# Kernel tuning notes

Measured on AMD Instinct MI355X. Metric: run time of the kernel, lower is better.

## Reference

```python
import jax, jax.numpy as jnp
import numpy as np

B, C, HH, WW, QK = 8, 64, 64, 64, 8


def setup_inputs() -> dict:
    key = jax.random.key(0)
    ks = jax.random.split(key, 22)
    s = 0.05
    def W(k, o, i):
        return jax.random.normal(k, (o, i), jnp.float32) * s
    def bvec(k, o):
        return jax.random.normal(k, (o,), jnp.float32) * s
    return {
        "H_in": jax.random.normal(ks[0], (B, C, HH, WW), jnp.float32),
        "M_prev": jax.random.normal(ks[1], (B, C, HH, WW), jnp.float32),
        "wq": W(ks[2], QK, C), "bq": bvec(ks[3], QK),
        "wkh": W(ks[4], QK, C), "bkh": bvec(ks[5], QK),
        "wvh": W(ks[6], C, C), "bvh": bvec(ks[7], C),
        "wkm": W(ks[8], QK, C), "bkm": bvec(ks[9], QK),
        "wvm": W(ks[10], C, C), "bvm": bvec(ks[11], C),
        "wz": W(ks[12], C, 2 * C), "bz": bvec(ks[13], C),
        "wo": W(ks[14], C, 2 * C), "bo": bvec(ks[15], C),
        "wg": W(ks[16], C, 2 * C), "bg": bvec(ks[17], C),
        "wi": W(ks[18], C, 2 * C), "bi": bvec(ks[19], C),
    }


def _conv1x1(w, b, x):
    # x: [B, Cin, N] -> [B, Cout, N]
    return jnp.einsum("oc,bcn->bon", w, x) + b[None, :, None]


def reference(H_in, M_prev, wq, bq, wkh, bkh, wvh, bvh, wkm, bkm, wvm, bvm,
              wz, bz, wo, bo, wg, bg, wi, bi):
    Bn, Cn, Hn, Wn = H_in.shape
    N = Hn * Wn
    h = H_in.reshape(Bn, Cn, N)   # flatten spatial
    m = M_prev.reshape(Bn, Cn, N)

    Q = _conv1x1(wq, bq, h)       # [B, QK, N]
    Kh = _conv1x1(wkh, bkh, h)
    Vh = _conv1x1(wvh, bvh, h)    # [B, C, N]
    Km = _conv1x1(wkm, bkm, m)
    Vm = _conv1x1(wvm, bvm, m)

    scale = jnp.asarray(np.sqrt(Q.shape[1]), Q.dtype)
    # scores: [B, N, N], softmax over last axis
    Ah = jax.nn.softmax(jnp.einsum("bcn,bcm->bnm", Q, Kh) / scale, axis=-1)
    Am = jax.nn.softmax(jnp.einsum("bcn,bcm->bnm", Q, Km) / scale, axis=-1)
    # Zh = Vh @ Ah^T : [B, C, N]
    Zh = jnp.einsum("bcm,bnm->bcn", Vh, Ah)
    Zm = jnp.einsum("bcm,bnm->bcn", Vm, Am)

    Z = _conv1x1(wz, bz, jnp.concatenate([Zh, Zm], axis=1))  # [B, C, N]
    concat = jnp.concatenate([h, Z], axis=1)                  # [B, 2C, N]
    O_t = jax.nn.sigmoid(_conv1x1(wo, bo, concat))
    G_t = jnp.tanh(_conv1x1(wg, bg, concat))
    I_t = jax.nn.sigmoid(_conv1x1(wi, bi, concat))

    M_t = (1.0 - I_t) * m + I_t * G_t
    H_out = O_t * M_t
    return (H_out.reshape(Bn, Cn, Hn, Wn), M_t.reshape(Bn, Cn, Hn, Wn))
```

## Files before the change

kernel.cpp:

```cpp
#include <hip/hip_runtime.h>

#define BATCH 8
#define CC 64
#define NN 4096
#define SCL 0.51006973f

typedef __attribute__((ext_vector_type(8))) short s16x8;
typedef __attribute__((ext_vector_type(4))) short s16x4;
typedef __attribute__((ext_vector_type(4))) float f32x4;
typedef __attribute__((ext_vector_type(2))) unsigned int uint2v;

__device__ __forceinline__ short f2bf(float f) {
  unsigned u = __builtin_bit_cast(unsigned, f);
  u += 0x7fffu + ((u >> 16) & 1u);
  return (short)(u >> 16);
}
__device__ __forceinline__ float bf2f(short h) {
  unsigned u = ((unsigned)(unsigned short)h) << 16;
  return __builtin_bit_cast(float, u);
}
__device__ __forceinline__ unsigned cvt_pk_bf16(float lo, float hi) {
  unsigned r;
  asm volatile("v_cvt_pk_bf16_f32 %0, %1, %2" : "=v"(r) : "v"(lo), "v"(hi));
  return r;
}

__device__ __forceinline__ int kperm(int kk) {
  int hh = (kk >> 5) & 1, g = (kk >> 3) & 3, c = kk & 7;
  return hh * 32 + (c < 4 ? (g << 2) + c : 16 + ((g ^ 2) << 2) + (c - 4));
}

__global__ void prep_weights_kernel(const float* __restrict__ wz, const float* __restrict__ bz,
                                    const float* __restrict__ wo, const float* __restrict__ bo,
                                    const float* __restrict__ wg, const float* __restrict__ bg,
                                    const float* __restrict__ wi, const float* __restrict__ bi,
                                    const float* __restrict__ wq, const float* __restrict__ bq,
                                    const float* __restrict__ wkh, const float* __restrict__ bkh,
                                    const float* __restrict__ wvh, const float* __restrict__ bvh,
                                    const float* __restrict__ wkm, const float* __restrict__ bkm,
                                    const float* __restrict__ wvm, const float* __restrict__ bvm,
                                    short* __restrict__ Weff, float* __restrict__ beff,
                                    short* __restrict__ Wcat, float* __restrict__ bias) {
  int i = blockIdx.x * 256 + threadIdx.x;
  const float* wjs[3] = {wo, wg, wi};
  const float* bjs[3] = {bo, bg, bi};
  const float gsc[3] = {1.44269504f, 2.88539008f, 1.44269504f};
  if (i < 36864) {
    int j = i / 12288, rem = i % 12288, o = rem / 192, k = rem % 192;
    const float* wj = wjs[j];
    float v;
    if (k < 64) {
      v = wj[o * 128 + k];
    } else {
      v = 0.f;
      #pragma unroll 8
      for (int t = 0; t < 64; ++t) v += wj[o * 128 + 64 + t] * wz[t * 128 + (k - 64)];
    }
    Weff[i] = f2bf(v * gsc[j]);
  } else if (i < 37056) {
    int i2 = i - 36864;
    int j = i2 >> 6, o = i2 & 63;
    const float* wj = wjs[j];
    float v = bjs[j][o];
    #pragma unroll 8
    for (int t = 0; t < 64; ++t) v += wj[o * 128 + 64 + t] * bz[t];
    beff[i2] = v * gsc[j];
  } else if (i < 47296) {
    int i2 = i - 37056;
    int src = i2 / 5120, rem = i2 % 5120, row = rem >> 6, col = rem & 63;
    float v;
    if (src == 0) {
      if (row < 64) v = wvh[row * 64 + col];
      else if (row < 72) v = wq[(row - 64) * 64 + col] * SCL;
      else v = wkh[(row - 72) * 64 + col];
    } else {
      if (row < 64) v = wvm[row * 64 + col];
      else if (row < 72) v = wkm[(row - 64) * 64 + col];
      else v = 0.f;
    }
    Wcat[i2] = f2bf(v);
  } else if (i < 47456) {
    int i3 = i - 47296;
    int src = i3 / 80, row = i3 % 80;
    float v;
    if (src == 0) v = (row < 64) ? bvh[row] : (row < 72 ? bq[row - 64] * SCL : bkh[row - 72]);
    else          v = (row < 64) ? bvm[row] : (row < 72 ? bkm[row - 64] : 0.f);
    bias[i3] = v;
  }
}

__global__ __launch_bounds__(256) void proj_kernel(
    const float* __restrict__ H_in, const float* __restrict__ M_prev,
    const short* __restrict__ Wcat, const float* __restrict__ bias,
    short* __restrict__ Qt, short* __restrict__ Kht, short* __restrict__ Kmt,
    short* __restrict__ Vh, short* __restrict__ Vm, short* __restrict__ Ht) {
  int src = blockIdx.x & 1;
  int n0 = ((blockIdx.x >> 1) & 31) << 7;
  int b = blockIdx.x >> 6;
  int tid = threadIdx.x, w = tid >> 6, l = tid & 63, lg = l >> 4, ll = l & 15;

  const float* __restrict__ X = src ? M_prev : H_in;
  short* __restrict__ Vp = src ? Vm : Vh;

  __shared__ __align__(16) short Xt[128][68];

  {
    int nl = tid & 127, chalf = (tid >> 7) << 5;
    int n = n0 + nl;
    #pragma unroll
    for (int cg = 0; cg < 8; ++cg) {
      int c = chalf + cg * 4;
      float v0 = X[((size_t)((b << 6) + c + 0)) * NN + n];
      float v1 = X[((size_t)((b << 6) + c + 1)) * NN + n];
      float v2 = X[((size_t)((b << 6) + c + 2)) * NN + n];
      float v3 = X[((size_t)((b << 6) + c + 3)) * NN + n];
      uint2v pk;
      pk.x = cvt_pk_bf16(v0, v1);
      pk.y = cvt_pk_bf16(v2, v3);
      *(uint2v*)&Xt[nl][c] = pk;
    }
  }
  __syncthreads();

  if (src == 0) {
    #pragma unroll
    for (int j = 0; j < 4; ++j) {
      int ci = tid + j * 256;
      int n = ci >> 3, seg = ci & 7;
      *(s16x8*)(Ht + ((size_t)(b * NN + n0 + n)) * 64 + seg * 8) = *(const s16x8*)&Xt[n][seg * 8];
    }
  }

  f32x4 acc[5][2];
  #pragma unroll
  for (int ot = 0; ot < 5; ++ot)
    #pragma unroll
    for (int ns = 0; ns < 2; ++ns)
      #pragma unroll
      for (int r = 0; r < 4; ++r) acc[ot][ns][r] = bias[src * 80 + ot * 16 + lg * 4 + r];

  #pragma unroll
  for (int kk = 0; kk < 2; ++kk) {
    s16x8 aw[5];
    #pragma unroll
    for (int ot = 0; ot < 5; ++ot)
      aw[ot] = *(const s16x8*)(Wcat + ((size_t)(src * 80 + ot * 16 + ll)) * 64 + kk * 32 + lg * 8);
    #pragma unroll
    for (int ns = 0; ns < 2; ++ns) {
      s16x8 bx = *(const s16x8*)&Xt[w * 32 + ns * 16 + ll][kk * 32 + lg * 8];
      #pragma unroll
      for (int ot = 0; ot < 5; ++ot)
        acc[ot][ns] = __builtin_amdgcn_mfma_f32_16x16x32_bf16(aw[ot], bx, acc[ot][ns], 0, 0, 0);
    }
  }

  #pragma unroll
  for (int ns = 0; ns < 2; ++ns) {
    int n = n0 + w * 32 + ns * 16 + ll;
    #pragma unroll
    for (int ot = 0; ot < 4; ++ot) {
      #pragma unroll
      for (int r = 0; r < 4; ++r) {
        int o = ot * 16 + lg * 4 + r;
        Vp[((size_t)((b << 6) + o)) * NN + n] = f2bf(acc[ot][ns][r]);
      }
    }
    int pr = (n & ~63) + kperm(n & 63);
    #pragma unroll
    for (int r = 0; r < 4; ++r) {
      float v = acc[4][ns][r];
      if (src == 0) {
        if (lg < 2) Qt[((size_t)(b * NN + n)) * 8 + (lg * 4 + r)] = f2bf(v);
        else        Kht[((size_t)(b * NN + pr)) * 8 + ((lg - 2) * 4 + r)] = f2bf(v);
      } else {
        if (lg < 2) Kmt[((size_t)(b * NN + pr)) * 8 + (lg * 4 + r)] = f2bf(v);
      }
    }
  }
}

__global__ __launch_bounds__(256, 6) void attn_kernel(
    const short* __restrict__ Qt, const short* __restrict__ Kht, const short* __restrict__ Kmt,
    const short* __restrict__ Vh, const short* __restrict__ Vm,
    short* __restrict__ Zp, float* __restrict__ dnb) {
  unsigned vb = (blockIdx.x & 7) * 256 + (blockIdx.x >> 3);
  int kh = vb >> 10;
  int b  = (vb >> 7) & 7;
  int s  = (vb >> 6) & 1;
  int q0 = (vb & 63) << 6;
  int tid = threadIdx.x;
  int w = tid >> 6, l = tid & 63, lg = l >> 4, ll = l & 15;
  const bool lo32 = (l < 32);

  const short* __restrict__ Kp = s ? Kmt : Kht;
  const short* __restrict__ Vp = s ? Vm : Vh;

  __shared__ __align__(16) short Vt[2][64][64];
  __shared__ __align__(16) short Ktl[2][64][8];
  short* VtF = &Vt[0][0][0];
  short* KtF = &Ktl[0][0][0];

  s16x8 bq = {};
  if (lg == 0) bq = *(const s16x8*)(Qt + ((size_t)(b * NN + q0 + w * 16 + ll)) * 8);
  s16x8 ones;
  #pragma unroll
  for (int i = 0; i < 8; ++i) ones[i] = (short)0x3F80;

  f32x4 accZ[4];
  f32x4 accDn = {0.f, 0.f, 0.f, 0.f};
  #pragma unroll
  for (int cs = 0; cs < 4; ++cs) accZ[cs] = (f32x4){0.f, 0.f, 0.f, 0.f};

  const int vOff0 = ll * 64 + ((lg ^ (ll & 7)) << 3);
  const int vOff1 = ll * 64 + (((lg ^ 4) ^ (ll & 7)) << 3);
  const int kOff  = ll * 8;

  const int row0 = w * 8 + (l >> 3);
  const int swz  = ((l & 7) ^ (l >> 3)) << 3;
  const short* vsrc0 = Vp + ((size_t)((b << 6) + row0)) * NN + kh * 2048 + swz;
  const short* vsrc1 = Vp + ((size_t)((b << 6) + 32 + row0)) * NN + kh * 2048 + swz;
  const short* ksrc  = Kp + ((size_t)(b * NN) + kh * 2048 + l) * 8;

#define GLDS(src_, dst_) \
  __builtin_amdgcn_global_load_lds((const __attribute__((address_space(1))) void*)(src_), \
                                   (__attribute__((address_space(3))) void*)(dst_), 16, 0, 0)
#define STAGE(bufL, ktL) do { \
    GLDS(vsrc0 + (ktL) * 64, VtF + (bufL) * 4096 + w * 512); \
    GLDS(vsrc1 + (ktL) * 64, VtF + (bufL) * 4096 + 2048 + w * 512); \
    if (w == 0) GLDS(ksrc + (ktL) * 512, KtF + (bufL) * 512); \
  } while (0)

  auto compute = [&](int bufL) {
    float p[4][4];
    #pragma unroll
    for (int hh = 0; hh < 2; ++hh) {
      #pragma unroll
      for (int par = 0; par < 2; ++par) {
        s16x8 ak = *(const s16x8*)(KtF + bufL * 512 + (hh * 32 + par * 16) * 8 + kOff);
        f32x4 sc = __builtin_amdgcn_mfma_f32_16x16x32_bf16(ak, bq, (f32x4){0.f,0.f,0.f,0.f}, 0, 0, 0);
        #pragma unroll
        for (int r = 0; r < 4; ++r) p[hh * 2 + par][r] = __builtin_amdgcn_exp2f(sc[r]);
      }
    }
    unsigned wkv[4][2];
    #pragma unroll
    for (int ks = 0; ks < 4; ++ks) {
      wkv[ks][0] = cvt_pk_bf16(p[ks][0], p[ks][1]);
      wkv[ks][1] = cvt_pk_bf16(p[ks][2], p[ks][3]);
    }
    #pragma unroll
    for (int hh = 0; hh < 2; ++hh) {
      unsigned o0 = wkv[hh * 2 + 1][0], o1 = wkv[hh * 2 + 1][1];
      uint2v pr0 = __builtin_amdgcn_permlane32_swap(o0, o0, false, false);
      uint2v pr1 = __builtin_amdgcn_permlane32_swap(o1, o1, false, false);
      unsigned sw0 = lo32 ? pr0.y : pr0.x;
      unsigned sw1 = lo32 ? pr1.y : pr1.x;
      union { unsigned u[4]; s16x8 v; } bpu;
      bpu.u[0] = wkv[hh * 2][0];
      bpu.u[1] = wkv[hh * 2][1];
      bpu.u[2] = sw0;
      bpu.u[3] = sw1;
      s16x8 bp = bpu.v;
      accDn = __builtin_amdgcn_mfma_f32_16x16x32_bf16(ones, bp, accDn, 0, 0, 0);
      const int vo = hh ? vOff1 : vOff0;
      #pragma unroll
      for (int cs = 0; cs < 4; ++cs) {
        s16x8 av = *(const s16x8*)(VtF + bufL * 4096 + cs * 1024 + vo);
        accZ[cs] = __builtin_amdgcn_mfma_f32_16x16x32_bf16(av, bp, accZ[cs], 0, 0, 0);
      }
    }
  };

  STAGE(0, 0);
  #pragma unroll 1
  for (int kt2 = 0; kt2 < 16; ++kt2) {
    int kt = kt2 * 2;
    asm volatile("s_waitcnt vmcnt(0)" ::: "memory");
    __builtin_amdgcn_s_barrier();
    STAGE(1, kt + 1);
    compute(0);
    asm volatile("s_waitcnt vmcnt(0)" ::: "memory");
    __builtin_amdgcn_s_barrier();
    if (kt2 < 15) STAGE(0, kt + 2);
    compute(1);
  }

  #pragma unroll
  for (int cs = 0; cs < 4; ++cs) {
    s16x4 o4;
    #pragma unroll
    for (int r = 0; r < 4; ++r) o4[r] = f2bf(accZ[cs][r]);
    *(s16x4*)(Zp + ((size_t)((kh * 8 + b) * NN + q0 + w * 16 + ll)) * 128 + s * 64 + cs * 16 + lg * 4) = o4;
  }
  if (l < 16)
    dnb[((size_t)(kh * 16 + b * 2 + s)) * NN + q0 + w * 16 + l] = accDn[0];
#undef STAGE
#undef GLDS
}

__global__ __launch_bounds__(256) void gates_kernel(
    const float* __restrict__ M_prev, const short* __restrict__ Ht,
    const short* __restrict__ Zp, const float* __restrict__ dnb,
    const short* __restrict__ Weff, const float* __restrict__ beff,
    float* __restrict__ out) {
  int b = blockIdx.x >> 7;
  int n0 = (blockIdx.x & 127) << 5;
  int tid = threadIdx.x, w = tid >> 6, l = tid & 63, lg = l >> 4, ll = l & 15;
  __shared__ __align__(16) short Xt[32][200];

  {
    int n = tid >> 3, seg = tid & 7;
    *(s16x8*)&Xt[n][seg * 8] = *(const s16x8*)(Ht + ((size_t)(b * NN + n0 + n)) * 64 + seg * 8);
  }
  {
    int n = tid >> 3, cq = tid & 7, sidx = cq >> 2;
    const short* z0 = Zp + ((size_t)(b * NN + n0 + n)) * 128 + cq * 16;
    const short* z1 = Zp + ((size_t)((8 + b) * NN + n0 + n)) * 128 + cq * 16;
    float d0 = dnb[((size_t)(b * 2 + sidx)) * NN + n0 + n];
    float d1 = dnb[((size_t)(16 + b * 2 + sidx)) * NN + n0 + n];
    float rd = __builtin_amdgcn_rcpf(d0 + d1);
    s16x8 a0 = *(const s16x8*)z0;
    s16x8 a1 = *(const s16x8*)z1;
    s16x8 b0 = *(const s16x8*)(z0 + 8);
    s16x8 b1 = *(const s16x8*)(z1 + 8);
    s16x8 o0, o1;
    #pragma unroll
    for (int j = 0; j < 8; ++j) {
      o0[j] = f2bf((bf2f(a0[j]) + bf2f(a1[j])) * rd);
      o1[j] = f2bf((bf2f(b0[j]) + bf2f(b1[j])) * rd);
    }
    *(s16x8*)&Xt[n][64 + cq * 16] = o0;
    *(s16x8*)&Xt[n][64 + cq * 16 + 8] = o1;
  }
  __syncthreads();

  f32x4 acc[3][2];
  #pragma unroll
  for (int j = 0; j < 3; ++j)
    #pragma unroll
    for (int ns = 0; ns < 2; ++ns)
      #pragma unroll
      for (int r = 0; r < 4; ++r) acc[j][ns][r] = beff[j * 64 + w * 16 + lg * 4 + r];

  #pragma unroll
  for (int kk = 0; kk < 6; ++kk) {
    s16x8 aw[3];
    #pragma unroll
    for (int j = 0; j < 3; ++j)
      aw[j] = *(const s16x8*)(Weff + ((size_t)(j * 64 + w * 16 + ll)) * 192 + kk * 32 + lg * 8);
    #pragma unroll
    for (int ns = 0; ns < 2; ++ns) {
      s16x8 bx = *(const s16x8*)&Xt[ns * 16 + ll][kk * 32 + lg * 8];
      #pragma unroll
      for (int j = 0; j < 3; ++j)
        acc[j][ns] = __builtin_amdgcn_mfma_f32_16x16x32_bf16(aw[j], bx, acc[j][ns], 0, 0, 0);
    }
  }

  float* Hout = out;
  float* Mout = out + (size_t)BATCH * CC * NN;
  #pragma unroll
  for (int ns = 0; ns < 2; ++ns) {
    #pragma unroll
    for (int r = 0; r < 4; ++r) {
      int c = w * 16 + lg * 4 + r;
      int n = n0 + ns * 16 + ll;
      size_t idx = ((size_t)((b << 6) + c)) * NN + n;
      float xo = acc[0][ns][r], xg = acc[1][ns][r], xi = acc[2][ns][r];
      float o  = __builtin_amdgcn_rcpf(1.f + __builtin_amdgcn_exp2f(-xo));
      float g  = 2.f * __builtin_amdgcn_rcpf(1.f + __builtin_amdgcn_exp2f(-xg)) - 1.f;
      float ii = __builtin_amdgcn_rcpf(1.f + __builtin_amdgcn_exp2f(-xi));
      float m  = M_prev[idx];
      float mt = (1.f - ii) * m + ii * g;
      Mout[idx] = mt;
      Hout[idx] = o * mt;
    }
  }
}

extern "C" void kernel_launch(void* const* d_in, const int* in_sizes, int n_in,
                              void* d_out, int out_size, void* d_ws, size_t ws_size,
                              hipStream_t stream) {
  (void)in_sizes; (void)n_in; (void)out_size; (void)ws_size;
  const float* H_in  = (const float*)d_in[0];
  const float* M_prev= (const float*)d_in[1];
  const float* wq  = (const float*)d_in[2];
  const float* bq  = (const float*)d_in[3];
  const float* wkh = (const float*)d_in[4];
  const float* bkh = (const float*)d_in[5];
  const float* wvh = (const float*)d_in[6];
  const float* bvh = (const float*)d_in[7];
  const float* wkm = (const float*)d_in[8];
  const float* bkm = (const float*)d_in[9];
  const float* wvm = (const float*)d_in[10];
  const float* bvm = (const float*)d_in[11];
  const float* wz  = (const float*)d_in[12];
  const float* bz  = (const float*)d_in[13];
  const float* wo  = (const float*)d_in[14];
  const float* bo  = (const float*)d_in[15];
  const float* wg  = (const float*)d_in[16];
  const float* bg  = (const float*)d_in[17];
  const float* wi  = (const float*)d_in[18];
  const float* bi  = (const float*)d_in[19];

  char* ws = (char*)d_ws;
  size_t off = 0;
  auto alloc = [&](size_t bytes) -> void* {
    void* p = ws + off;
    off += (bytes + 255) & ~(size_t)255;
    return p;
  };
  short* Weff = (short*)alloc(3 * 64 * 192 * 2);
  float* beff = (float*)alloc(192 * 4);
  short* Wcat = (short*)alloc(2 * 80 * 64 * 2);
  float* bias = (float*)alloc(160 * 4);
  short* Qt   = (short*)alloc((size_t)BATCH * NN * 8 * 2);
  short* Kht  = (short*)alloc((size_t)BATCH * NN * 8 * 2);
  short* Kmt  = (short*)alloc((size_t)BATCH * NN * 8 * 2);
  short* Vh   = (short*)alloc((size_t)BATCH * CC * NN * 2);
  short* Vm   = (short*)alloc((size_t)BATCH * CC * NN * 2);
  short* Ht   = (short*)alloc((size_t)BATCH * NN * 64 * 2);
  short* Zp   = (short*)alloc((size_t)2 * BATCH * NN * 128 * 2);
  float* dnb  = (float*)alloc((size_t)2 * BATCH * 2 * NN * 4);

  prep_weights_kernel<<<186, 256, 0, stream>>>(wz, bz, wo, bo, wg, bg, wi, bi,
                                               wq, bq, wkh, bkh, wvh, bvh, wkm, bkm, wvm, bvm,
                                               Weff, beff, Wcat, bias);
  proj_kernel<<<512, 256, 0, stream>>>(H_in, M_prev, Wcat, bias, Qt, Kht, Kmt, Vh, Vm, Ht);
  attn_kernel<<<2048, 256, 0, stream>>>(Qt, Kht, Kmt, Vh, Vm, Zp, dnb);
  gates_kernel<<<1024, 256, 0, stream>>>(M_prev, Ht, Zp, dnb, Weff, beff, (float*)d_out);
}
```

Measured before the change: 189.7 us.

## Vectorize projection I/O via LDS staging, drop Ht buffer, raise attn occupancy

The projection kernel now handles 64-column tiles with 1024 blocks. It reads inputs as float4 and transposes them into LDS. Its V outputs are staged through a shared tile so they go out as 16-byte coalesced stores instead of scattered 2-byte writes. The bf16 copy of H (Ht) is removed, and the gates kernel re-reads H_in in fp32 and converts it itself. The attention kernel's launch bounds are raised to 8 waves/blocks per SM, which trades register budget for occupancy and risks spills.

```diff
diff --git a/kernel.cpp b/kernel.cpp
--- a/kernel.cpp
+++ b/kernel.cpp
@@ -93,82 +93,60 @@
     const float* __restrict__ H_in, const float* __restrict__ M_prev,
     const short* __restrict__ Wcat, const float* __restrict__ bias,
     short* __restrict__ Qt, short* __restrict__ Kht, short* __restrict__ Kmt,
-    short* __restrict__ Vh, short* __restrict__ Vm, short* __restrict__ Ht) {
+    short* __restrict__ Vh, short* __restrict__ Vm) {
   int src = blockIdx.x & 1;
-  int n0 = ((blockIdx.x >> 1) & 31) << 7;
-  int b = blockIdx.x >> 6;
+  int n0 = ((blockIdx.x >> 1) & 63) << 6;
+  int b = blockIdx.x >> 7;
   int tid = threadIdx.x, w = tid >> 6, l = tid & 63, lg = l >> 4, ll = l & 15;
 
   const float* __restrict__ X = src ? M_prev : H_in;
   short* __restrict__ Vp = src ? Vm : Vh;
 
-  __shared__ __align__(16) short Xt[128][68];
+  __shared__ __align__(16) short Xt[64][68];
+  __shared__ __align__(16) short Ot[64][76];
 
   {
-    int nl = tid & 127, chalf = (tid >> 7) << 5;
-    int n = n0 + nl;
-    #pragma unroll
-    for (int cg = 0; cg < 8; ++cg) {
-      int c = chalf + cg * 4;
-      float v0 = X[((size_t)((b << 6) + c + 0)) * NN + n];
-      float v1 = X[((size_t)((b << 6) + c + 1)) * NN + n];
-      float v2 = X[((size_t)((b << 6) + c + 2)) * NN + n];
-      float v3 = X[((size_t)((b << 6) + c + 3)) * NN + n];
-      uint2v pk;
-      pk.x = cvt_pk_bf16(v0, v1);
-      pk.y = cvt_pk_bf16(v2, v3);
-      *(uint2v*)&Xt[nl][c] = pk;
+    int c = tid & 63, q = tid >> 6;
+    const float* xs = X + ((size_t)((b << 6) + c)) * NN + n0 + q * 16;
+    #pragma unroll
+    for (int j = 0; j < 4; ++j) {
+      float4 v = *(const float4*)(xs + j * 4);
+      Xt[q * 16 + j * 4 + 0][c] = f2bf(v.x);
+      Xt[q * 16 + j * 4 + 1][c] = f2bf(v.y);
+      Xt[q * 16 + j * 4 + 2][c] = f2bf(v.z);
+      Xt[q * 16 + j * 4 + 3][c] = f2bf(v.w);
     }
   }
   __syncthreads();
 
-  if (src == 0) {
-    #pragma unroll
-    for (int j = 0; j < 4; ++j) {
-      int ci = tid + j * 256;
-      int n = ci >> 3, seg = ci & 7;
-      *(s16x8*)(Ht + ((size_t)(b * NN + n0 + n)) * 64 + seg * 8) = *(const s16x8*)&Xt[n][seg * 8];
-    }
-  }
-
-  f32x4 acc[5][2];
+  f32x4 acc[5];
   #pragma unroll
   for (int ot = 0; ot < 5; ++ot)
     #pragma unroll
-    for (int ns = 0; ns < 2; ++ns)
-      #pragma unroll
-      for (int r = 0; r < 4; ++r) acc[ot][ns][r] = bias[src * 80 + ot * 16 + lg * 4 + r];
+    for (int r = 0; r < 4; ++r) acc[ot][r] = bias[src * 80 + ot * 16 + lg * 4 + r];
 
   #pragma unroll
   for (int kk = 0; kk < 2; ++kk) {
-    s16x8 aw[5];
-    #pragma unroll
-    for (int ot = 0; ot < 5; ++ot)
-      aw[ot] = *(const s16x8*)(Wcat + ((size_t)(src * 80 + ot * 16 + ll)) * 64 + kk * 32 + lg * 8);
-    #pragma unroll
-    for (int ns = 0; ns < 2; ++ns) {
-      s16x8 bx = *(const s16x8*)&Xt[w * 32 + ns * 16 + ll][kk * 32 + lg * 8];
-      #pragma unroll
-      for (int ot = 0; ot < 5; ++ot)
-        acc[ot][ns] = __builtin_amdgcn_mfma_f32_16x16x32_bf16(aw[ot], bx, acc[ot][ns], 0, 0, 0);
-    }
-  }
-
-  #pragma unroll
-  for (int ns = 0; ns < 2; ++ns) {
-    int n = n0 + w * 32 + ns * 16 + ll;
-    #pragma unroll
-    for (int ot = 0; ot < 4; ++ot) {
-      #pragma unroll
-      for (int r = 0; r < 4; ++r) {
-        int o = ot * 16 + lg * 4 + r;
-        Vp[((size_t)((b << 6) + o)) * NN + n] = f2bf(acc[ot][ns][r]);
-      }
-    }
+    s16x8 bx = *(const s16x8*)&Xt[w * 16 + ll][kk * 32 + lg * 8];
+    #pragma unroll
+    for (int ot = 0; ot < 5; ++ot) {
+      s16x8 aw = *(const s16x8*)(Wcat + ((size_t)(src * 80 + ot * 16 + ll)) * 64 + kk * 32 + lg * 8);
+      acc[ot] = __builtin_amdgcn_mfma_f32_16x16x32_bf16(aw, bx, acc[ot], 0, 0, 0);
+    }
+  }
+
+  #pragma unroll
+  for (int ot = 0; ot < 4; ++ot)
+    #pragma unroll
+    for (int r = 0; r < 4; ++r)
+      Ot[ot * 16 + lg * 4 + r][w * 16 + ll] = f2bf(acc[ot][r]);
+
+  {
+    int n = n0 + w * 16 + ll;
     int pr = (n & ~63) + kperm(n & 63);
     #pragma unroll
     for (int r = 0; r < 4; ++r) {
-      float v = acc[4][ns][r];
+      float v = acc[4][r];
       if (src == 0) {
         if (lg < 2) Qt[((size_t)(b * NN + n)) * 8 + (lg * 4 + r)] = f2bf(v);
         else        Kht[((size_t)(b * NN + pr)) * 8 + ((lg - 2) * 4 + r)] = f2bf(v);
@@ -177,9 +155,18 @@
       }
     }
   }
-}
-
-__global__ __launch_bounds__(256, 6) void attn_kernel(
+  __syncthreads();
+
+  #pragma unroll
+  for (int h = 0; h < 2; ++h) {
+    int ci = tid + h * 256;
+    int row = ci >> 3, seg = ci & 7;
+    *(s16x8*)(Vp + ((size_t)((b << 6) + row)) * NN + n0 + seg * 8) =
+        *(const s16x8*)&Ot[row][seg * 8];
+  }
+}
+
+__global__ __launch_bounds__(256, 8) void attn_kernel(
     const short* __restrict__ Qt, const short* __restrict__ Kht, const short* __restrict__ Kmt,
     const short* __restrict__ Vh, const short* __restrict__ Vm,
     short* __restrict__ Zp, float* __restrict__ dnb) {
@@ -299,7 +286,7 @@
 }
 
 __global__ __launch_bounds__(256) void gates_kernel(
-    const float* __restrict__ M_prev, const short* __restrict__ Ht,
+    const float* __restrict__ H_in, const float* __restrict__ M_prev,
     const short* __restrict__ Zp, const float* __restrict__ dnb,
     const short* __restrict__ Weff, const float* __restrict__ beff,
     float* __restrict__ out) {
@@ -309,8 +296,16 @@
   __shared__ __align__(16) short Xt[32][200];
 
   {
-    int n = tid >> 3, seg = tid & 7;
-    *(s16x8*)&Xt[n][seg * 8] = *(const s16x8*)(Ht + ((size_t)(b * NN + n0 + n)) * 64 + seg * 8);
+    int c = tid & 63, q = tid >> 6;
+    const float* xs = H_in + ((size_t)((b << 6) + c)) * NN + n0 + q * 8;
+    #pragma unroll
+    for (int j = 0; j < 2; ++j) {
+      float4 v = *(const float4*)(xs + j * 4);
+      Xt[q * 8 + j * 4 + 0][c] = f2bf(v.x);
+      Xt[q * 8 + j * 4 + 1][c] = f2bf(v.y);
+      Xt[q * 8 + j * 4 + 2][c] = f2bf(v.z);
+      Xt[q * 8 + j * 4 + 3][c] = f2bf(v.w);
+    }
   }
   {
     int n = tid >> 3, cq = tid & 7, sidx = cq >> 2;
@@ -419,14 +414,13 @@
   short* Kmt  = (short*)alloc((size_t)BATCH * NN * 8 * 2);
   short* Vh   = (short*)alloc((size_t)BATCH * CC * NN * 2);
   short* Vm   = (short*)alloc((size_t)BATCH * CC * NN * 2);
-  short* Ht   = (short*)alloc((size_t)BATCH * NN * 64 * 2);
   short* Zp   = (short*)alloc((size_t)2 * BATCH * NN * 128 * 2);
   float* dnb  = (float*)alloc((size_t)2 * BATCH * 2 * NN * 4);
 
   prep_weights_kernel<<<186, 256, 0, stream>>>(wz, bz, wo, bo, wg, bg, wi, bi,
                                                wq, bq, wkh, bkh, wvh, bvh, wkm, bkm, wvm, bvm,
                                                Weff, beff, Wcat, bias);
-  proj_kernel<<<512, 256, 0, stream>>>(H_in, M_prev, Wcat, bias, Qt, Kht, Kmt, Vh, Vm, Ht);
+  proj_kernel<<<1024, 256, 0, stream>>>(H_in, M_prev, Wcat, bias, Qt, Kht, Kmt, Vh, Vm);
   attn_kernel<<<2048, 256, 0, stream>>>(Qt, Kht, Kmt, Vh, Vm, Zp, dnb);
-  gates_kernel<<<1024, 256, 0, stream>>>(M_prev, Ht, Zp, dnb, Weff, beff, (float*)d_out);
-}
+  gates_kernel<<<1024, 256, 0, stream>>>(H_in, M_prev, Zp, dnb, Weff, beff, (float*)d_out);
+}
```

New measurement: 191.4 us. Within noise of the previous version (+0.9%).
